# Optimization experiments

Measured on AMD Instinct MI355X. Metric: run time of the kernel, lower is better.

Reference implementation:

```python
import jax, jax.numpy as jnp
import numpy as np

N_NODES = 50000
EPS = 1e-7      # GENConv message epsilon
BN_EPS = 1e-5   # BatchNorm1d eps
N_AGGR = 2


def setup_inputs() -> dict:
    key = jax.random.key(0)
    ks = jax.random.split(key, 8)
    C = 64
    E = 800000
    x = jax.random.normal(ks[0], (N_NODES, C), dtype=jnp.float32)
    edge_index = jax.random.randint(ks[1], (2, E), 0, N_NODES, dtype=jnp.int64)
    # per-GENConv MLP params, stacked over the N_AGGR layers
    W1 = jax.random.normal(ks[2], (N_AGGR, C, 2 * C), dtype=jnp.float32) * (1.0 / np.sqrt(C))
    b1 = jnp.zeros((N_AGGR, 2 * C), dtype=jnp.float32)
    gamma = jnp.ones((N_AGGR, 2 * C), dtype=jnp.float32)
    beta = jnp.zeros((N_AGGR, 2 * C), dtype=jnp.float32)
    W2 = jax.random.normal(ks[3], (N_AGGR, 2 * C, C), dtype=jnp.float32) * (1.0 / np.sqrt(2 * C))
    b2 = jnp.zeros((N_AGGR, C), dtype=jnp.float32)
    t = jnp.ones((N_AGGR,), dtype=jnp.float32)  # learnable softmax temperature
    return {"x": x, "edge_index": edge_index, "W1": W1, "b1": b1,
            "gamma": gamma, "beta": beta, "W2": W2, "b2": b2, "t": t}


def _gen_conv(x, src, dst, W1_l, b1_l, gamma_l, beta_l, W2_l, b2_l, t_l):
    # message: relu(x_j) + eps  (edge_attr is None)
    m = jax.nn.relu(x[src]) + EPS                      # [E, C]
    # softmax aggregation over edges grouped by destination node
    logits = m * t_l                                   # [E, C]
    seg_max = jax.ops.segment_max(logits, dst, num_segments=N_NODES)  # [N, C]
    ex = jnp.exp(logits - seg_max[dst])                # [E, C]
    den = jax.ops.segment_sum(ex, dst, num_segments=N_NODES)          # [N, C]
    alpha = ex / (den[dst] + 1e-16)                    # [E, C]
    aggr = jax.ops.segment_sum(m * alpha, dst, num_segments=N_NODES)  # [N, C]
    # residual then MLP: Linear(C,2C) -> BatchNorm1d (train-mode stats) -> ReLU -> Linear(2C,C)
    h = aggr + x
    h = h @ W1_l + b1_l                                # [N, 2C]
    mean = h.mean(axis=0)
    var = h.var(axis=0)                                # biased variance (torch BN)
    h = (h - mean) / jnp.sqrt(var + BN_EPS) * gamma_l + beta_l
    h = jax.nn.relu(h)
    h = h @ W2_l + b2_l                                # [N, C]
    return h


def reference(x, edge_index, W1, b1, gamma, beta, W2, b2, t):
    src = edge_index[0]
    dst = edge_index[1]
    for l in range(N_AGGR):
        x = _gen_conv(x, src, dst, W1[l], b1[l], gamma[l], beta[l], W2[l], b2[l], t[l])
        x = jax.nn.relu(x)
        # dropout in eval mode == identity
    return x
```

## Files before the change

kernel.cpp:

```cpp
#include <hip/hip_runtime.h>
#include <math.h>

#define NN 50000
#define EPSM 1e-7f
#define BN_EPS 1e-5f
#define NBK 391
#define LOG2E 1.44269504088896340736f


__global__ __launch_bounds__(256) void bucket_hist_kernel(
    const int* __restrict__ dst, int* __restrict__ bhist, int E,
    unsigned* __restrict__ mm0, float* __restrict__ bn0){
  __shared__ int h[NBK];
  int t = threadIdx.x;
  if (blockIdx.x == 0){
    if (t < 64) mm0[t] = 0x7F7FFFFFu;
    else if (t < 128) mm0[t] = 0u;
    bn0[t] = 0.f;
  }
  for (int i = t; i < NBK; i += 256) h[i] = 0;
  __syncthreads();
  int e0 = blockIdx.x * 4096;
  int cnt = min(4096, E - e0);
  for (int i = t; i < cnt; i += 256) atomicAdd(&h[dst[e0 + i] >> 7], 1);
  __syncthreads();
  for (int i = t; i < NBK; i += 256) if (h[i]) atomicAdd(&bhist[i], h[i]);
}

__global__ void bucket_scan_kernel(const int* __restrict__ bhist,
                                   int* __restrict__ bbase, int* __restrict__ gcur){
  int lane = threadIdx.x;
  int loc[7]; int s = 0;
#pragma unroll
  for (int k = 0; k < 7; ++k){
    int i = lane * 7 + k;
    int v = (i < NBK) ? bhist[i] : 0;
    loc[k] = s; s += v;
  }
  int sc = s;
#pragma unroll
  for (int o = 1; o < 64; o <<= 1){
    int n = __shfl_up(sc, o);
    if (lane >= o) sc += n;
  }
  int exc = sc - s;
#pragma unroll
  for (int k = 0; k < 7; ++k){
    int i = lane * 7 + k;
    if (i < NBK){ bbase[i] = exc + loc[k]; gcur[i] = exc + loc[k]; }
    else if (i == NBK) bbase[i] = exc + loc[k];
  }
}

__global__ __launch_bounds__(256) void bucket_scatter_kernel(
    const int* __restrict__ src, const int* __restrict__ dst,
    int* __restrict__ gcur, unsigned* __restrict__ packed_g, int E){
  __shared__ int hist[NBK], offs[NBK], gb[NBK], curk[NBK];
  __shared__ unsigned stage[4096];
  __shared__ int gpos[4096];
  int t = threadIdx.x;
  for (int i = t; i < NBK; i += 256) hist[i] = 0;
  __syncthreads();
  int e0 = blockIdx.x * 4096;
  int cnt = min(4096, E - e0);
  unsigned pk[16]; int bk[16];
  int nmine = 0;
  for (int i = t; i < cnt; i += 256){
    int d = dst[e0 + i], s = src[e0 + i];
    pk[nmine] = ((unsigned)d << 16) | (unsigned)s;
    bk[nmine] = d >> 7;
    atomicAdd(&hist[bk[nmine]], 1);
    ++nmine;
  }
  __syncthreads();
  if (t < 64){
    int loc[7]; int s = 0;
#pragma unroll
    for (int k = 0; k < 7; ++k){
      int i = t * 7 + k;
      int v = (i < NBK) ? hist[i] : 0;
      loc[k] = s; s += v;
    }
    int sc = s;
#pragma unroll
    for (int o = 1; o < 64; o <<= 1){
      int n = __shfl_up(sc, o);
      if (t >= o) sc += n;
    }
    int exc = sc - s;
#pragma unroll
    for (int k = 0; k < 7; ++k){
      int i = t * 7 + k;
      if (i < NBK) offs[i] = exc + loc[k];
    }
  }
  __syncthreads();
  for (int i = t; i < NBK; i += 256){
    int h = hist[i];
    gb[i] = h ? atomicAdd(&gcur[i], h) : 0;
    curk[i] = offs[i];
  }
  __syncthreads();
  for (int k = 0; k < nmine; ++k){
    int b = bk[k];
    int p = atomicAdd(&curk[b], 1);
    stage[p] = pk[k];
    gpos[p] = gb[b] + (p - offs[b]);
  }
  __syncthreads();
  for (int j = t; j < cnt; j += 256) packed_g[gpos[j]] = stage[j];
}

__global__ __launch_bounds__(256) void bucket_place_kernel(
    const unsigned* __restrict__ packed_g, const int* __restrict__ bbase,
    int* __restrict__ start_g, int* __restrict__ end_g,
    unsigned short* __restrict__ srcs_g, int N){
  __shared__ int deg[128], off[128], cur[128];
  __shared__ int sstage[4096];
  int b = blockIdx.x, t = threadIdx.x;
  int beg = bbase[b], cnt = bbase[b + 1] - beg;
  if (t < 128) deg[t] = 0;
  __syncthreads();
  for (int j = t; j < cnt; j += 256)
    atomicAdd(&deg[(packed_g[beg + j] >> 16) & 127], 1);
  __syncthreads();
  if (t < 64){
    int i0 = t * 2;
    int v0 = deg[i0], v1 = deg[i0 + 1];
    int s = v0 + v1;
    int sc = s;
#pragma unroll
    for (int o = 1; o < 64; o <<= 1){
      int n = __shfl_up(sc, o);
      if (t >= o) sc += n;
    }
    int exc = sc - s;
    off[i0] = exc; off[i0 + 1] = exc + v0;
  }
  __syncthreads();
  int node0 = b * 128;
  if (t < 128){
    int node = node0 + t;
    if (node < N){
      start_g[node] = beg + off[t];
      end_g[node] = beg + off[t] + deg[t];
    }
    cur[t] = off[t];
  }
  __syncthreads();
  if (cnt <= 4096){
    for (int j = t; j < cnt; j += 256){
      unsigned p = packed_g[beg + j];
      int lp = atomicAdd(&cur[(p >> 16) & 127], 1);
      sstage[lp] = (int)(p & 0xFFFFu);
    }
    __syncthreads();
    for (int j = t; j < cnt; j += 256)
      srcs_g[beg + j] = (unsigned short)sstage[j];
  } else {
    for (int j = t; j < cnt; j += 256){
      unsigned p = packed_g[beg + j];
      int lp = atomicAdd(&cur[(p >> 16) & 127], 1);
      srcs_g[beg + lp] = (unsigned short)(p & 0xFFFFu);
    }
  }
}


__global__ __launch_bounds__(256) void colminmax_kernel(
    const float* __restrict__ x, unsigned* __restrict__ mm,
    unsigned short* __restrict__ mh, int N){
  __shared__ unsigned smn[256], smx[256];
  int c = threadIdx.x & 63;
  int slot = blockIdx.x * 4 + (threadIdx.x >> 6);
  float mx = 0.f, mn = 1e30f;
  for (int r = slot; r < N; r += 256 * 4){
    float m = fmaxf(x[r * 64 + c], 0.f) + EPSM;
    unsigned u = __float_as_uint(m);
    u += 0x7FFFu + ((u >> 16) & 1u);
    unsigned short us = (unsigned short)(u >> 16);
    mh[r * 64 + c] = us;
    float mb = __uint_as_float(((unsigned)us) << 16);
    mx = fmaxf(mx, mb);
    mn = fminf(mn, mb);
  }
  smn[threadIdx.x] = __float_as_uint(mn);
  smx[threadIdx.x] = __float_as_uint(mx);
  __syncthreads();
  if (threadIdx.x < 64){
    unsigned a = smn[c], b = smn[c + 64], d = smn[c + 128], e = smn[c + 192];
    atomicMin(&mm[c], min(min(a, b), min(d, e)));
    a = smx[c]; b = smx[c + 64]; d = smx[c + 128]; e = smx[c + 192];
    atomicMax(&mm[64 + c], max(max(a, b), max(d, e)));
  }
}


__global__ __launch_bounds__(256) void aggregate_kernel(
    const float* __restrict__ x, const unsigned* __restrict__ mh32,
    const int* __restrict__ start, const int* __restrict__ segend,
    const unsigned short* __restrict__ srcs, const float* __restrict__ tptr,
    int layer, const unsigned* __restrict__ mm, float* __restrict__ h0, int N){
  int node = blockIdx.x * 4 + (threadIdx.x >> 6);
  if (node >= N) return;
  int lane = threadIdx.x & 63;
  int half = lane >> 5, cp = lane & 31;
  float t2 = tptr[layer] * LOG2E;
  float mnL = __uint_as_float(mm[2 * cp]);
  float mxL = __uint_as_float(mm[64 + 2 * cp]);
  float mnH = __uint_as_float(mm[2 * cp + 1]);
  float mxH = __uint_as_float(mm[64 + 2 * cp + 1]);
  float BL = fmaxf(t2 * mxL, t2 * mnL);
  float BH = fmaxf(t2 * mxH, t2 * mnH);
  int beg = start[node], end = segend[node];
  float dL0=0.f,dL1=0.f,dL2=0.f,dL3=0.f, nL0=0.f,nL1=0.f,nL2=0.f,nL3=0.f;
  float dH0=0.f,dH1=0.f,dH2=0.f,dH3=0.f, nH0=0.f,nH1=0.f,nH2=0.f,nH3=0.f;
  int e = beg + half;
  for (; e + 6 < end; e += 8){
    int s0 = srcs[e], s1 = srcs[e + 2], s2 = srcs[e + 4], s3 = srcs[e + 6];
    unsigned u0 = mh32[s0 * 32 + cp], u1 = mh32[s1 * 32 + cp];
    unsigned u2 = mh32[s2 * 32 + cp], u3 = mh32[s3 * 32 + cp];
    float mL0 = __uint_as_float(u0 << 16), mH0 = __uint_as_float(u0 & 0xFFFF0000u);
    float mL1 = __uint_as_float(u1 << 16), mH1 = __uint_as_float(u1 & 0xFFFF0000u);
    float mL2 = __uint_as_float(u2 << 16), mH2 = __uint_as_float(u2 & 0xFFFF0000u);
    float mL3 = __uint_as_float(u3 << 16), mH3 = __uint_as_float(u3 & 0xFFFF0000u);
    float pL0 = exp2f(mL0 * t2 - BL), pH0 = exp2f(mH0 * t2 - BH);
    float pL1 = exp2f(mL1 * t2 - BL), pH1 = exp2f(mH1 * t2 - BH);
    float pL2 = exp2f(mL2 * t2 - BL), pH2 = exp2f(mH2 * t2 - BH);
    float pL3 = exp2f(mL3 * t2 - BL), pH3 = exp2f(mH3 * t2 - BH);
    dL0 += pL0; nL0 += mL0 * pL0;  dH0 += pH0; nH0 += mH0 * pH0;
    dL1 += pL1; nL1 += mL1 * pL1;  dH1 += pH1; nH1 += mH1 * pH1;
    dL2 += pL2; nL2 += mL2 * pL2;  dH2 += pH2; nH2 += mH2 * pH2;
    dL3 += pL3; nL3 += mL3 * pL3;  dH3 += pH3; nH3 += mH3 * pH3;
  }
  for (; e < end; e += 2){
    int s = srcs[e];
    unsigned u = mh32[s * 32 + cp];
    float mL = __uint_as_float(u << 16), mH = __uint_as_float(u & 0xFFFF0000u);
    float pL = exp2f(mL * t2 - BL), pH = exp2f(mH * t2 - BH);
    dL0 += pL; nL0 += mL * pL;  dH0 += pH; nH0 += mH * pH;
  }
  float dL = (dL0 + dL1) + (dL2 + dL3), nL = (nL0 + nL1) + (nL2 + nL3);
  float dH = (dH0 + dH1) + (dH2 + dH3), nH = (nH0 + nH1) + (nH2 + nH3);
  dL += __shfl_xor(dL, 32); nL += __shfl_xor(nL, 32);
  dH += __shfl_xor(dH, 32); nH += __shfl_xor(nH, 32);
  if (half == 0){
    float2 xv = ((const float2*)x)[node * 32 + cp];
    float2 o;
    o.x = nL / (dL + 1e-16f) + xv.x;
    o.y = nH / (dH + 1e-16f) + xv.y;
    ((float2*)h0)[node * 32 + cp] = o;
  }
}


__global__ __launch_bounds__(256) void gemm1_kernel(
    const float* __restrict__ h0, const float* __restrict__ W1,
    const float* __restrict__ b1, float* __restrict__ h1,
    float* __restrict__ bn, int N,
    unsigned* __restrict__ mm_next, float* __restrict__ bn_next){
  __shared__ float a_lds[64 * 68];
  __shared__ float w_lds[64 * 128];
  int t = threadIdx.x;
  if (mm_next != 0 && blockIdx.x == 0){
    if (t < 64) mm_next[t] = 0x7F7FFFFFu;
    else if (t < 128) mm_next[t] = 0u;
    bn_next[t] = 0.f;
  }
  const float4* wg = (const float4*)W1;
  float4* wl = (float4*)w_lds;
#pragma unroll
  for (int i = 0; i < 8; ++i) wl[t + 256 * i] = wg[t + 256 * i];
  int row0 = blockIdx.x * 64;
#pragma unroll
  for (int i = 0; i < 4; ++i){
    int li = t + 256 * i;
    int r = li >> 4, q = li & 15;
    int gr = row0 + r;
    float4 v = make_float4(0.f, 0.f, 0.f, 0.f);
    if (gr < N) v = ((const float4*)h0)[gr * 16 + q];
    *(float4*)&a_lds[r * 68 + q * 4] = v;
  }
  __syncthreads();
  int tc = t & 31, tr = t >> 5;
  float4 bias = ((const float4*)b1)[tc];
  float acc[8][4];
#pragma unroll
  for (int r = 0; r < 8; ++r){
    acc[r][0] = bias.x; acc[r][1] = bias.y; acc[r][2] = bias.z; acc[r][3] = bias.w;
  }
  for (int k = 0; k < 64; k += 4){
    float4 w0 = *(const float4*)&w_lds[(k + 0) * 128 + tc * 4];
    float4 w1 = *(const float4*)&w_lds[(k + 1) * 128 + tc * 4];
    float4 w2 = *(const float4*)&w_lds[(k + 2) * 128 + tc * 4];
    float4 w3 = *(const float4*)&w_lds[(k + 3) * 128 + tc * 4];
#pragma unroll
    for (int r = 0; r < 8; ++r){
      float4 a = *(const float4*)&a_lds[(tr * 8 + r) * 68 + k];
      acc[r][0] += a.x * w0.x + a.y * w1.x + a.z * w2.x + a.w * w3.x;
      acc[r][1] += a.x * w0.y + a.y * w1.y + a.z * w2.y + a.w * w3.y;
      acc[r][2] += a.x * w0.z + a.y * w1.z + a.z * w2.z + a.w * w3.z;
      acc[r][3] += a.x * w0.w + a.y * w1.w + a.z * w2.w + a.w * w3.w;
    }
  }
  float s[4] = {0.f, 0.f, 0.f, 0.f}, s2[4] = {0.f, 0.f, 0.f, 0.f};
#pragma unroll
  for (int r = 0; r < 8; ++r){
    int gr = row0 + tr * 8 + r;
    if (gr < N){
      *(float4*)&h1[gr * 128 + tc * 4] =
          make_float4(acc[r][0], acc[r][1], acc[r][2], acc[r][3]);
#pragma unroll
      for (int j = 0; j < 4; ++j){ s[j] += acc[r][j]; s2[j] += acc[r][j] * acc[r][j]; }
    }
  }
  __syncthreads();
  float* red = a_lds;
  if (t < 256){ red[t] = 0.f; }
  __syncthreads();
#pragma unroll
  for (int j = 0; j < 4; ++j){
    atomicAdd(&red[tc * 4 + j], s[j]);
    atomicAdd(&red[128 + tc * 4 + j], s2[j]);
  }
  __syncthreads();
  if (t < 256) atomicAdd(&bn[t], red[t]);
}

__global__ __launch_bounds__(256) void gemm2_kernel(
    const float* __restrict__ h1, const float* __restrict__ bn,
    const float* __restrict__ gamma, const float* __restrict__ beta, int layer,
    const float* __restrict__ W2, const float* __restrict__ b2,
    float* __restrict__ xout, int N,
    unsigned* __restrict__ mm_next, unsigned short* __restrict__ mh_next){
  __shared__ float a_lds[64 * 132];
  __shared__ float w_lds[128 * 68];
  __shared__ float ss[256];
  __shared__ unsigned smn[64], smx[64];
  int t = threadIdx.x;
  if (t < 128){
    float mean = bn[t] * (1.f / (float)N);
    float var = bn[128 + t] * (1.f / (float)N) - mean * mean;
    var = fmaxf(var, 0.f);
    float sc = gamma[layer * 128 + t] / sqrtf(var + BN_EPS);
    ss[t] = sc;
    ss[128 + t] = beta[layer * 128 + t] - mean * sc;
  }
  if (t < 64){ smn[t] = 0x7F7FFFFFu; smx[t] = 0u; }
  const float4* wg = (const float4*)W2;
#pragma unroll
  for (int i = 0; i < 8; ++i){
    int li = t + 256 * i;
    int k = li >> 4, q = li & 15;
    *(float4*)&w_lds[k * 68 + q * 4] = wg[li];
  }
  __syncthreads();
  int row0 = blockIdx.x * 64;
#pragma unroll
  for (int i = 0; i < 8; ++i){
    int li = t + 256 * i;
    int r = li >> 5, q = li & 31;
    int gr = row0 + r;
    float4 v = make_float4(0.f, 0.f, 0.f, 0.f);
    if (gr < N) v = ((const float4*)h1)[gr * 32 + q];
    float4 sc = *(const float4*)&ss[q * 4];
    float4 sh = *(const float4*)&ss[128 + q * 4];
    v.x = fmaxf(v.x * sc.x + sh.x, 0.f);
    v.y = fmaxf(v.y * sc.y + sh.y, 0.f);
    v.z = fmaxf(v.z * sc.z + sh.z, 0.f);
    v.w = fmaxf(v.w * sc.w + sh.w, 0.f);
    *(float4*)&a_lds[r * 132 + q * 4] = v;
  }
  __syncthreads();
  int tc = t & 15, tr = t >> 4;
  float4 bias = ((const float4*)b2)[tc];
  float acc[4][4];
#pragma unroll
  for (int r = 0; r < 4; ++r){
    acc[r][0] = bias.x; acc[r][1] = bias.y; acc[r][2] = bias.z; acc[r][3] = bias.w;
  }
  for (int k = 0; k < 128; k += 4){
    float4 w0 = *(const float4*)&w_lds[(k + 0) * 68 + tc * 4];
    float4 w1 = *(const float4*)&w_lds[(k + 1) * 68 + tc * 4];
    float4 w2 = *(const float4*)&w_lds[(k + 2) * 68 + tc * 4];
    float4 w3 = *(const float4*)&w_lds[(k + 3) * 68 + tc * 4];
#pragma unroll
    for (int r = 0; r < 4; ++r){
      float4 a = *(const float4*)&a_lds[(tr * 4 + r) * 132 + k];
      acc[r][0] += a.x * w0.x + a.y * w1.x + a.z * w2.x + a.w * w3.x;
      acc[r][1] += a.x * w0.y + a.y * w1.y + a.z * w2.y + a.w * w3.y;
      acc[r][2] += a.x * w0.z + a.y * w1.z + a.z * w2.z + a.w * w3.z;
      acc[r][3] += a.x * w0.w + a.y * w1.w + a.z * w2.w + a.w * w3.w;
    }
  }
  unsigned mnv[4] = {0x7F7FFFFFu, 0x7F7FFFFFu, 0x7F7FFFFFu, 0x7F7FFFFFu};
  unsigned mxv[4] = {0u, 0u, 0u, 0u};
#pragma unroll
  for (int r = 0; r < 4; ++r){
    int gr = row0 + tr * 4 + r;
    if (gr < N){
      float o0 = fmaxf(acc[r][0], 0.f), o1 = fmaxf(acc[r][1], 0.f);
      float o2 = fmaxf(acc[r][2], 0.f), o3 = fmaxf(acc[r][3], 0.f);
      *(float4*)&xout[gr * 64 + tc * 4] = make_float4(o0, o1, o2, o3);
      if (mh_next != 0){
        unsigned us[4];
        float ov[4] = {o0, o1, o2, o3};
#pragma unroll
        for (int j = 0; j < 4; ++j){
          unsigned u = __float_as_uint(ov[j] + EPSM);
          u += 0x7FFFu + ((u >> 16) & 1u);
          us[j] = u >> 16;
          unsigned fb = us[j] << 16;
          mnv[j] = min(mnv[j], fb);
          mxv[j] = max(mxv[j], fb);
        }
        ((uint2*)mh_next)[gr * 16 + tc] =
            make_uint2(us[0] | (us[1] << 16), us[2] | (us[3] << 16));
      }
    }
  }
  if (mh_next != 0){
    __syncthreads();
#pragma unroll
    for (int j = 0; j < 4; ++j){
      atomicMin(&smn[tc * 4 + j], mnv[j]);
      atomicMax(&smx[tc * 4 + j], mxv[j]);
    }
    __syncthreads();
    if (t < 64){
      atomicMin(&mm_next[t], smn[t]);
      atomicMax(&mm_next[64 + t], smx[t]);
    }
  }
}

extern "C" void kernel_launch(void* const* d_in, const int* in_sizes, int n_in,
                              void* d_out, int out_size, void* d_ws, size_t ws_size,
                              hipStream_t stream) {
  const float* x0    = (const float*)d_in[0];
  const int*   ei    = (const int*)d_in[1];
  const float* W1    = (const float*)d_in[2];
  const float* b1    = (const float*)d_in[3];
  const float* gamma = (const float*)d_in[4];
  const float* beta  = (const float*)d_in[5];
  const float* W2    = (const float*)d_in[6];
  const float* b2    = (const float*)d_in[7];
  const float* tptr  = (const float*)d_in[8];

  const int N = NN;
  const int E = in_sizes[1] / 2;
  const int* src = ei;
  const int* dst = ei + E;

  float* ws  = (float*)d_ws;
  float* h0  = ws;
  float* h1  = h0 + N * 64;
  float* bn0 = h1 + N * 128;
  float* bn1 = bn0 + 256;
  unsigned* mm0 = (unsigned*)(bn1 + 256);
  unsigned* mm1 = mm0 + 128;
  unsigned short* mh = (unsigned short*)(mm1 + 128);
  int* bhist = (int*)(mh + N * 64);
  int* bbase = bhist + NBK;
  int* gcur  = bbase + NBK + 1;
  int* start = gcur + NBK;
  int* segend = start + N;
  unsigned* packed = (unsigned*)(segend + N);
  unsigned short* srcs = (unsigned short*)(packed + E);

  float* out = (float*)d_out;

  const int row_blocks = (N + 63) / 64;
  const int chunk_blocks = (E + 4095) / 4096;
  const int agg_blocks = (N + 3) / 4;

  hipMemsetAsync(bhist, 0, NBK * sizeof(int), stream);
  bucket_hist_kernel<<<chunk_blocks, 256, 0, stream>>>(dst, bhist, E, mm0, bn0);
  bucket_scan_kernel<<<1, 64, 0, stream>>>(bhist, bbase, gcur);
  bucket_scatter_kernel<<<chunk_blocks, 256, 0, stream>>>(src, dst, gcur, packed, E);
  bucket_place_kernel<<<NBK, 256, 0, stream>>>(packed, bbase, start, segend, srcs, N);

  colminmax_kernel<<<256, 256, 0, stream>>>(x0, mm0, mh, N);
  aggregate_kernel<<<agg_blocks, 256, 0, stream>>>(x0, (const unsigned*)mh, start,
                                                   segend, srcs, tptr, 0, mm0, h0, N);
  gemm1_kernel<<<row_blocks, 256, 0, stream>>>(h0, W1, b1, h1, bn0, N, mm1, bn1);
  gemm2_kernel<<<row_blocks, 256, 0, stream>>>(h1, bn0, gamma, beta, 0, W2, b2,
                                               out, N, mm1, mh);
  aggregate_kernel<<<agg_blocks, 256, 0, stream>>>(out, (const unsigned*)mh, start,
                                                   segend, srcs, tptr, 1, mm1, h0, N);
  gemm1_kernel<<<row_blocks, 256, 0, stream>>>(h0, W1 + 8192, b1 + 128, h1, bn1, N,
                                               (unsigned*)0, (float*)0);
  gemm2_kernel<<<row_blocks, 256, 0, stream>>>(h1, bn1, gamma, beta, 1, W2 + 8192,
                                               b2 + 64, out, N,
                                               (unsigned*)0, (unsigned short*)0);
}
```

Baseline: 335.4 us.

## Fuse aggregation into GEMM1 and merge histogram with column min/max pass

The softmax aggregation now writes its residual-added rows straight into shared memory, and the first linear layer consumes them in the same 512-thread kernel. This removes the h0 round trip through global memory and one launch per layer. The bucket histogram and the bf16 message/min-max pass share one kernel, and workspace initialisation moves to memsets. In exchange, each block now pairs irregular gather work with a GEMM, which may lower occupancy or cause load imbalance across waves.

```diff
diff --git a/kernel.cpp b/kernel.cpp
--- a/kernel.cpp
+++ b/kernel.cpp
@@ -8,23 +8,44 @@
 #define LOG2E 1.44269504088896340736f
 
 
-__global__ __launch_bounds__(256) void bucket_hist_kernel(
+__global__ __launch_bounds__(256) void hist_cmm_kernel(
     const int* __restrict__ dst, int* __restrict__ bhist, int E,
-    unsigned* __restrict__ mm0, float* __restrict__ bn0){
+    const float* __restrict__ x, unsigned* __restrict__ mm,
+    unsigned short* __restrict__ mh, int N){
   __shared__ int h[NBK];
+  __shared__ unsigned smn[256], smx[256];
   int t = threadIdx.x;
-  if (blockIdx.x == 0){
-    if (t < 64) mm0[t] = 0x7F7FFFFFu;
-    else if (t < 128) mm0[t] = 0u;
-    bn0[t] = 0.f;
-  }
-  for (int i = t; i < NBK; i += 256) h[i] = 0;
-  __syncthreads();
-  int e0 = blockIdx.x * 4096;
-  int cnt = min(4096, E - e0);
-  for (int i = t; i < cnt; i += 256) atomicAdd(&h[dst[e0 + i] >> 7], 1);
-  __syncthreads();
-  for (int i = t; i < NBK; i += 256) if (h[i]) atomicAdd(&bhist[i], h[i]);
+  int nchunks = (E + 4095) >> 12;
+  if ((int)blockIdx.x < nchunks){
+    for (int i = t; i < NBK; i += 256) h[i] = 0;
+    __syncthreads();
+    int e0 = blockIdx.x * 4096;
+    int cnt = min(4096, E - e0);
+    for (int i = t; i < cnt; i += 256) atomicAdd(&h[dst[e0 + i] >> 7], 1);
+    __syncthreads();
+    for (int i = t; i < NBK; i += 256) if (h[i]) atomicAdd(&bhist[i], h[i]);
+  }
+  int c = t & 63;
+  float mx = 0.f, mn = 1e30f;
+  for (int r = blockIdx.x * 4 + (t >> 6); r < N; r += gridDim.x * 4){
+    float m = fmaxf(x[r * 64 + c], 0.f) + EPSM;
+    unsigned u = __float_as_uint(m);
+    u += 0x7FFFu + ((u >> 16) & 1u);
+    unsigned short us = (unsigned short)(u >> 16);
+    mh[r * 64 + c] = us;
+    float mb = __uint_as_float(((unsigned)us) << 16);
+    mx = fmaxf(mx, mb);
+    mn = fminf(mn, mb);
+  }
+  smn[t] = __float_as_uint(mn);
+  smx[t] = __float_as_uint(mx);
+  __syncthreads();
+  if (t < 64){
+    unsigned a = smn[c], b = smn[c + 64], d = smn[c + 128], e = smn[c + 192];
+    atomicMin(&mm[c], min(min(a, b), min(d, e)));
+    a = smx[c]; b = smx[c + 64]; d = smx[c + 128]; e = smx[c + 192];
+    atomicMax(&mm[64 + c], max(max(a, b), max(d, e)));
+  }
 }
 
 __global__ void bucket_scan_kernel(const int* __restrict__ bhist,
@@ -167,44 +188,28 @@
 }
 
 
-__global__ __launch_bounds__(256) void colminmax_kernel(
-    const float* __restrict__ x, unsigned* __restrict__ mm,
-    unsigned short* __restrict__ mh, int N){
-  __shared__ unsigned smn[256], smx[256];
-  int c = threadIdx.x & 63;
-  int slot = blockIdx.x * 4 + (threadIdx.x >> 6);
-  float mx = 0.f, mn = 1e30f;
-  for (int r = slot; r < N; r += 256 * 4){
-    float m = fmaxf(x[r * 64 + c], 0.f) + EPSM;
-    unsigned u = __float_as_uint(m);
-    u += 0x7FFFu + ((u >> 16) & 1u);
-    unsigned short us = (unsigned short)(u >> 16);
-    mh[r * 64 + c] = us;
-    float mb = __uint_as_float(((unsigned)us) << 16);
-    mx = fmaxf(mx, mb);
-    mn = fminf(mn, mb);
-  }
-  smn[threadIdx.x] = __float_as_uint(mn);
-  smx[threadIdx.x] = __float_as_uint(mx);
-  __syncthreads();
-  if (threadIdx.x < 64){
-    unsigned a = smn[c], b = smn[c + 64], d = smn[c + 128], e = smn[c + 192];
-    atomicMin(&mm[c], min(min(a, b), min(d, e)));
-    a = smx[c]; b = smx[c + 64]; d = smx[c + 128]; e = smx[c + 192];
-    atomicMax(&mm[64 + c], max(max(a, b), max(d, e)));
-  }
-}
-
-
-__global__ __launch_bounds__(256) void aggregate_kernel(
+__global__ __launch_bounds__(512) void agg_gemm1_kernel(
     const float* __restrict__ x, const unsigned* __restrict__ mh32,
     const int* __restrict__ start, const int* __restrict__ segend,
     const unsigned short* __restrict__ srcs, const float* __restrict__ tptr,
-    int layer, const unsigned* __restrict__ mm, float* __restrict__ h0, int N){
-  int node = blockIdx.x * 4 + (threadIdx.x >> 6);
-  if (node >= N) return;
-  int lane = threadIdx.x & 63;
-  int half = lane >> 5, cp = lane & 31;
+    int layer, const unsigned* __restrict__ mm,
+    const float* __restrict__ W1, const float* __restrict__ b1,
+    float* __restrict__ h1, float* __restrict__ bn, int N,
+    unsigned* __restrict__ mm_next, float* __restrict__ bn_next){
+  __shared__ float a_lds[64 * 68];
+  __shared__ float w_lds[64 * 128];
+  int t = threadIdx.x;
+  if (mm_next != 0 && blockIdx.x == 0){
+    if (t < 64) mm_next[t] = 0x7F7FFFFFu;
+    else if (t < 128) mm_next[t] = 0u;
+    if (t < 256) bn_next[t] = 0.f;
+  }
+  const float4* wg = (const float4*)W1;
+  float4* wl = (float4*)w_lds;
+#pragma unroll
+  for (int i = 0; i < 4; ++i) wl[t + 512 * i] = wg[t + 512 * i];
+
+  int wv = t >> 6, lane = t & 63, half = lane >> 5, cp = lane & 31;
   float t2 = tptr[layer] * LOG2E;
   float mnL = __uint_as_float(mm[2 * cp]);
   float mxL = __uint_as_float(mm[64 + 2 * cp]);
@@ -212,81 +217,60 @@
   float mxH = __uint_as_float(mm[64 + 2 * cp + 1]);
   float BL = fmaxf(t2 * mxL, t2 * mnL);
   float BH = fmaxf(t2 * mxH, t2 * mnH);
-  int beg = start[node], end = segend[node];
-  float dL0=0.f,dL1=0.f,dL2=0.f,dL3=0.f, nL0=0.f,nL1=0.f,nL2=0.f,nL3=0.f;
-  float dH0=0.f,dH1=0.f,dH2=0.f,dH3=0.f, nH0=0.f,nH1=0.f,nH2=0.f,nH3=0.f;
-  int e = beg + half;
-  for (; e + 6 < end; e += 8){
-    int s0 = srcs[e], s1 = srcs[e + 2], s2 = srcs[e + 4], s3 = srcs[e + 6];
-    unsigned u0 = mh32[s0 * 32 + cp], u1 = mh32[s1 * 32 + cp];
-    unsigned u2 = mh32[s2 * 32 + cp], u3 = mh32[s3 * 32 + cp];
-    float mL0 = __uint_as_float(u0 << 16), mH0 = __uint_as_float(u0 & 0xFFFF0000u);
-    float mL1 = __uint_as_float(u1 << 16), mH1 = __uint_as_float(u1 & 0xFFFF0000u);
-    float mL2 = __uint_as_float(u2 << 16), mH2 = __uint_as_float(u2 & 0xFFFF0000u);
-    float mL3 = __uint_as_float(u3 << 16), mH3 = __uint_as_float(u3 & 0xFFFF0000u);
-    float pL0 = exp2f(mL0 * t2 - BL), pH0 = exp2f(mH0 * t2 - BH);
-    float pL1 = exp2f(mL1 * t2 - BL), pH1 = exp2f(mH1 * t2 - BH);
-    float pL2 = exp2f(mL2 * t2 - BL), pH2 = exp2f(mH2 * t2 - BH);
-    float pL3 = exp2f(mL3 * t2 - BL), pH3 = exp2f(mH3 * t2 - BH);
-    dL0 += pL0; nL0 += mL0 * pL0;  dH0 += pH0; nH0 += mH0 * pH0;
-    dL1 += pL1; nL1 += mL1 * pL1;  dH1 += pH1; nH1 += mH1 * pH1;
-    dL2 += pL2; nL2 += mL2 * pL2;  dH2 += pH2; nH2 += mH2 * pH2;
-    dL3 += pL3; nL3 += mL3 * pL3;  dH3 += pH3; nH3 += mH3 * pH3;
-  }
-  for (; e < end; e += 2){
-    int s = srcs[e];
-    unsigned u = mh32[s * 32 + cp];
-    float mL = __uint_as_float(u << 16), mH = __uint_as_float(u & 0xFFFF0000u);
-    float pL = exp2f(mL * t2 - BL), pH = exp2f(mH * t2 - BH);
-    dL0 += pL; nL0 += mL * pL;  dH0 += pH; nH0 += mH * pH;
-  }
-  float dL = (dL0 + dL1) + (dL2 + dL3), nL = (nL0 + nL1) + (nL2 + nL3);
-  float dH = (dH0 + dH1) + (dH2 + dH3), nH = (nH0 + nH1) + (nH2 + nH3);
-  dL += __shfl_xor(dL, 32); nL += __shfl_xor(nL, 32);
-  dH += __shfl_xor(dH, 32); nH += __shfl_xor(nH, 32);
-  if (half == 0){
-    float2 xv = ((const float2*)x)[node * 32 + cp];
-    float2 o;
-    o.x = nL / (dL + 1e-16f) + xv.x;
-    o.y = nH / (dH + 1e-16f) + xv.y;
-    ((float2*)h0)[node * 32 + cp] = o;
-  }
-}
-
-
-__global__ __launch_bounds__(256) void gemm1_kernel(
-    const float* __restrict__ h0, const float* __restrict__ W1,
-    const float* __restrict__ b1, float* __restrict__ h1,
-    float* __restrict__ bn, int N,
-    unsigned* __restrict__ mm_next, float* __restrict__ bn_next){
-  __shared__ float a_lds[64 * 68];
-  __shared__ float w_lds[64 * 128];
-  int t = threadIdx.x;
-  if (mm_next != 0 && blockIdx.x == 0){
-    if (t < 64) mm_next[t] = 0x7F7FFFFFu;
-    else if (t < 128) mm_next[t] = 0u;
-    bn_next[t] = 0.f;
-  }
-  const float4* wg = (const float4*)W1;
-  float4* wl = (float4*)w_lds;
-#pragma unroll
-  for (int i = 0; i < 8; ++i) wl[t + 256 * i] = wg[t + 256 * i];
   int row0 = blockIdx.x * 64;
-#pragma unroll
-  for (int i = 0; i < 4; ++i){
-    int li = t + 256 * i;
-    int r = li >> 4, q = li & 15;
-    int gr = row0 + r;
-    float4 v = make_float4(0.f, 0.f, 0.f, 0.f);
-    if (gr < N) v = ((const float4*)h0)[gr * 16 + q];
-    *(float4*)&a_lds[r * 68 + q * 4] = v;
-  }
-  __syncthreads();
+#pragma unroll 1
+  for (int i = 0; i < 8; ++i){
+    int row = wv * 8 + i;
+    int node = row0 + row;
+    if (node < N){
+      int beg = start[node], end = segend[node];
+      float dL0=0.f,dL1=0.f,dL2=0.f,dL3=0.f, nL0=0.f,nL1=0.f,nL2=0.f,nL3=0.f;
+      float dH0=0.f,dH1=0.f,dH2=0.f,dH3=0.f, nH0=0.f,nH1=0.f,nH2=0.f,nH3=0.f;
+      int e = beg + half;
+      for (; e + 6 < end; e += 8){
+        int s0 = srcs[e], s1 = srcs[e + 2], s2 = srcs[e + 4], s3 = srcs[e + 6];
+        unsigned u0 = mh32[s0 * 32 + cp], u1 = mh32[s1 * 32 + cp];
+        unsigned u2 = mh32[s2 * 32 + cp], u3 = mh32[s3 * 32 + cp];
+        float mL0 = __uint_as_float(u0 << 16), mH0 = __uint_as_float(u0 & 0xFFFF0000u);
+        float mL1 = __uint_as_float(u1 << 16), mH1 = __uint_as_float(u1 & 0xFFFF0000u);
+        float mL2 = __uint_as_float(u2 << 16), mH2 = __uint_as_float(u2 & 0xFFFF0000u);
+        float mL3 = __uint_as_float(u3 << 16), mH3 = __uint_as_float(u3 & 0xFFFF0000u);
+        float pL0 = exp2f(mL0 * t2 - BL), pH0 = exp2f(mH0 * t2 - BH);
+        float pL1 = exp2f(mL1 * t2 - BL), pH1 = exp2f(mH1 * t2 - BH);
+        float pL2 = exp2f(mL2 * t2 - BL), pH2 = exp2f(mH2 * t2 - BH);
+        float pL3 = exp2f(mL3 * t2 - BL), pH3 = exp2f(mH3 * t2 - BH);
+        dL0 += pL0; nL0 += mL0 * pL0;  dH0 += pH0; nH0 += mH0 * pH0;
+        dL1 += pL1; nL1 += mL1 * pL1;  dH1 += pH1; nH1 += mH1 * pH1;
+        dL2 += pL2; nL2 += mL2 * pL2;  dH2 += pH2; nH2 += mH2 * pH2;
+        dL3 += pL3; nL3 += mL3 * pL3;  dH3 += pH3; nH3 += mH3 * pH3;
+      }
+      for (; e < end; e += 2){
+        int s = srcs[e];
+        unsigned u = mh32[s * 32 + cp];
+        float mL = __uint_as_float(u << 16), mH = __uint_as_float(u & 0xFFFF0000u);
+        float pL = exp2f(mL * t2 - BL), pH = exp2f(mH * t2 - BH);
+        dL0 += pL; nL0 += mL * pL;  dH0 += pH; nH0 += mH * pH;
+      }
+      float dL = (dL0 + dL1) + (dL2 + dL3), nL = (nL0 + nL1) + (nL2 + nL3);
+      float dH = (dH0 + dH1) + (dH2 + dH3), nH = (nH0 + nH1) + (nH2 + nH3);
+      dL += __shfl_xor(dL, 32); nL += __shfl_xor(nL, 32);
+      dH += __shfl_xor(dH, 32); nH += __shfl_xor(nH, 32);
+      if (half == 0){
+        float2 xv = ((const float2*)x)[node * 32 + cp];
+        *(float2*)&a_lds[row * 68 + 2 * cp] =
+            make_float2(nL / (dL + 1e-16f) + xv.x, nH / (dH + 1e-16f) + xv.y);
+      }
+    } else if (half == 0){
+      *(float2*)&a_lds[row * 68 + 2 * cp] = make_float2(0.f, 0.f);
+    }
+  }
+  __syncthreads();
+
   int tc = t & 31, tr = t >> 5;
   float4 bias = ((const float4*)b1)[tc];
-  float acc[8][4];
-#pragma unroll
-  for (int r = 0; r < 8; ++r){
+  float acc[4][4];
+#pragma unroll
+  for (int r = 0; r < 4; ++r){
     acc[r][0] = bias.x; acc[r][1] = bias.y; acc[r][2] = bias.z; acc[r][3] = bias.w;
   }
   for (int k = 0; k < 64; k += 4){
@@ -295,8 +279,8 @@
     float4 w2 = *(const float4*)&w_lds[(k + 2) * 128 + tc * 4];
     float4 w3 = *(const float4*)&w_lds[(k + 3) * 128 + tc * 4];
 #pragma unroll
-    for (int r = 0; r < 8; ++r){
-      float4 a = *(const float4*)&a_lds[(tr * 8 + r) * 68 + k];
+    for (int r = 0; r < 4; ++r){
+      float4 a = *(const float4*)&a_lds[(tr * 4 + r) * 68 + k];
       acc[r][0] += a.x * w0.x + a.y * w1.x + a.z * w2.x + a.w * w3.x;
       acc[r][1] += a.x * w0.y + a.y * w1.y + a.z * w2.y + a.w * w3.y;
       acc[r][2] += a.x * w0.z + a.y * w1.z + a.z * w2.z + a.w * w3.z;
@@ -305,8 +289,8 @@
   }
   float s[4] = {0.f, 0.f, 0.f, 0.f}, s2[4] = {0.f, 0.f, 0.f, 0.f};
 #pragma unroll
-  for (int r = 0; r < 8; ++r){
-    int gr = row0 + tr * 8 + r;
+  for (int r = 0; r < 4; ++r){
+    int gr = row0 + tr * 4 + r;
     if (gr < N){
       *(float4*)&h1[gr * 128 + tc * 4] =
           make_float4(acc[r][0], acc[r][1], acc[r][2], acc[r][3]);
@@ -453,15 +437,14 @@
   const int* dst = ei + E;
 
   float* ws  = (float*)d_ws;
-  float* h0  = ws;
-  float* h1  = h0 + N * 64;
-  float* bn0 = h1 + N * 128;
-  float* bn1 = bn0 + 256;
-  unsigned* mm0 = (unsigned*)(bn1 + 256);
-  unsigned* mm1 = mm0 + 128;
-  unsigned short* mh = (unsigned short*)(mm1 + 128);
-  int* bhist = (int*)(mh + N * 64);
-  int* bbase = bhist + NBK;
+  float* h1  = ws;
+  unsigned* mm0 = (unsigned*)(h1 + N * 128);
+  float* bn0 = (float*)(mm0 + 128);
+  int* bhist = (int*)(bn0 + 256);
+  unsigned* mm1 = (unsigned*)(bhist + NBK);
+  float* bn1 = (float*)(mm1 + 128);
+  unsigned short* mh = (unsigned short*)(bn1 + 256);
+  int* bbase = (int*)(mh + N * 64);
   int* gcur  = bbase + NBK + 1;
   int* start = gcur + NBK;
   int* segend = start + N;
@@ -472,24 +455,25 @@
 
   const int row_blocks = (N + 63) / 64;
   const int chunk_blocks = (E + 4095) / 4096;
-  const int agg_blocks = (N + 3) / 4;
-
-  hipMemsetAsync(bhist, 0, NBK * sizeof(int), stream);
-  bucket_hist_kernel<<<chunk_blocks, 256, 0, stream>>>(dst, bhist, E, mm0, bn0);
+  const int hc_blocks = chunk_blocks > 256 ? chunk_blocks : 256;
+
+  hipMemsetAsync(mm0, 0xFF, 64 * sizeof(unsigned), stream);
+  hipMemsetAsync(mm0 + 64, 0, (64 + 256 + NBK) * sizeof(unsigned), stream);
+
+  hist_cmm_kernel<<<hc_blocks, 256, 0, stream>>>(dst, bhist, E, x0, mm0, mh, N);
   bucket_scan_kernel<<<1, 64, 0, stream>>>(bhist, bbase, gcur);
   bucket_scatter_kernel<<<chunk_blocks, 256, 0, stream>>>(src, dst, gcur, packed, E);
   bucket_place_kernel<<<NBK, 256, 0, stream>>>(packed, bbase, start, segend, srcs, N);
 
-  colminmax_kernel<<<256, 256, 0, stream>>>(x0, mm0, mh, N);
-  aggregate_kernel<<<agg_blocks, 256, 0, stream>>>(x0, (const unsigned*)mh, start,
-                                                   segend, srcs, tptr, 0, mm0, h0, N);
-  gemm1_kernel<<<row_blocks, 256, 0, stream>>>(h0, W1, b1, h1, bn0, N, mm1, bn1);
+  agg_gemm1_kernel<<<row_blocks, 512, 0, stream>>>(x0, (const unsigned*)mh, start,
+                                                   segend, srcs, tptr, 0, mm0,
+                                                   W1, b1, h1, bn0, N, mm1, bn1);
   gemm2_kernel<<<row_blocks, 256, 0, stream>>>(h1, bn0, gamma, beta, 0, W2, b2,
                                                out, N, mm1, mh);
-  aggregate_kernel<<<agg_blocks, 256, 0, stream>>>(out, (const unsigned*)mh, start,
-                                                   segend, srcs, tptr, 1, mm1, h0, N);
-  gemm1_kernel<<<row_blocks, 256, 0, stream>>>(h0, W1 + 8192, b1 + 128, h1, bn1, N,
-                                               (unsigned*)0, (float*)0);
+  agg_gemm1_kernel<<<row_blocks, 512, 0, stream>>>(out, (const unsigned*)mh, start,
+                                                   segend, srcs, tptr, 1, mm1,
+                                                   W1 + 8192, b1 + 128, h1, bn1, N,
+                                                   (unsigned*)0, (float*)0);
   gemm2_kernel<<<row_blocks, 256, 0, stream>>>(h1, bn1, gamma, beta, 1, W2 + 8192,
                                                b2 + 64, out, N,
                                                (unsigned*)0, (unsigned short*)0);
```

Result: slower. 1.136 ms (+238.7%).
